# Kernel optimization log

Measured on AMD Instinct MI355X. Metric: run time of the kernel, lower is better.

The kernel has to match this reference:

```python
import jax, jax.numpy as jnp
import numpy as np

NEG_SLOPE = 0.2
BN_EPS = 1e-5
SM_EPS = 1e-16


def gatv2_conv(x, src, dst, num_nodes, Wl, bl, Wr, br, att, bias, concat):
    # x: [N, Fin]; att: [H, C]
    H, C = att.shape
    xl = (x @ Wl + bl).reshape(-1, H, C)  # source-side (x_j), lin_l
    xr = (x @ Wr + br).reshape(-1, H, C)  # target-side (x_i), lin_r
    e = jax.nn.leaky_relu(xl[src] + xr[dst], NEG_SLOPE)          # [E, H, C]
    logits = jnp.einsum('ehc,hc->eh', e, att)                    # [E, H]
    m = jax.ops.segment_max(logits, dst, num_segments=num_nodes)  # [N, H]
    expv = jnp.exp(logits - m[dst])
    denom = jax.ops.segment_sum(expv, dst, num_segments=num_nodes)
    alpha = expv / (denom[dst] + SM_EPS)                          # [E, H]
    msg = xl[src] * alpha[:, :, None]                             # [E, H, C]
    out = jax.ops.segment_sum(msg, dst, num_segments=num_nodes)   # [N, H, C]
    out = out.reshape(num_nodes, H * C) if concat else out.mean(axis=1)
    return out + bias


def batchnorm(x, gamma, beta):
    mean = x.mean(axis=0)
    var = x.var(axis=0)  # biased, as torch uses for normalization
    return gamma * (x - mean) * jax.lax.rsqrt(var + BN_EPS) + beta


def setup_inputs() -> dict:
    key = jax.random.key(0)
    ks = jax.random.split(key, 16)
    N, E = 50000, 800000
    Fin, Hid, Out, H = 128, 64, 64, 4
    s = 0.05
    inp = {
        'x': jax.random.normal(ks[0], (N, Fin), jnp.float32),
        'edge_index': jax.random.randint(ks[1], (2, E), 0, N, jnp.int64),
        # conv1 (heads=4, concat=False)
        'Wl1': jax.random.normal(ks[2], (Fin, H * Hid), jnp.float32) * s,
        'bl1': jnp.zeros((H * Hid,), jnp.float32),
        'Wr1': jax.random.normal(ks[3], (Fin, H * Hid), jnp.float32) * s,
        'br1': jnp.zeros((H * Hid,), jnp.float32),
        'att1': jax.random.normal(ks[4], (H, Hid), jnp.float32) * s,
        'bias1': jnp.zeros((Hid,), jnp.float32),
        'g1': jnp.ones((Hid,), jnp.float32),
        'beta1': jnp.zeros((Hid,), jnp.float32),
        # conv2 (heads=1, concat=True -> same as single head)
        'Wl2': jax.random.normal(ks[5], (Hid, Out), jnp.float32) * s,
        'bl2': jnp.zeros((Out,), jnp.float32),
        'Wr2': jax.random.normal(ks[6], (Hid, Out), jnp.float32) * s,
        'br2': jnp.zeros((Out,), jnp.float32),
        'att2': jax.random.normal(ks[7], (1, Out), jnp.float32) * s,
        'bias2': jnp.zeros((Out,), jnp.float32),
        'g2': jnp.ones((Out,), jnp.float32),
        'beta2': jnp.zeros((Out,), jnp.float32),
    }
    return inp


def reference(x, edge_index, Wl1, bl1, Wr1, br1, att1, bias1, g1, beta1,
              Wl2, bl2, Wr2, br2, att2, bias2, g2, beta2):
    N = x.shape[0]
    loops = jnp.arange(N, dtype=edge_index.dtype)  # PyG add_self_loops=True
    src = jnp.concatenate([edge_index[0], loops])
    dst = jnp.concatenate([edge_index[1], loops])
    h = gatv2_conv(x, src, dst, N, Wl1, bl1, Wr1, br1, att1, bias1, concat=False)
    h = jax.nn.relu(batchnorm(h, g1, beta1))  # dropout = identity (eval)
    h = gatv2_conv(h, src, dst, N, Wl2, bl2, Wr2, br2, att2, bias2, concat=True)
    h = jax.nn.relu(batchnorm(h, g2, beta2))
    return h
```

## Files before the change

kernel.cpp:

```cpp
#include <hip/hip_runtime.h>
#include <hip/hip_bf16.h>
#include <math.h>

#define TPB 256

typedef __attribute__((ext_vector_type(8))) short bfrag8;
typedef __attribute__((ext_vector_type(4))) float f32x4;

static __device__ __forceinline__ float bf2f(unsigned int u) {
  union { unsigned int i; float f; } c; c.i = u << 16; return c.f;
}
static __device__ __forceinline__ unsigned short f2bf(float f) {
  union { float f; unsigned int i; } c; c.f = f;
  unsigned int lsb = (c.i >> 16) & 1u;
  return (unsigned short)((c.i + 0x7fffu + lsb) >> 16);
}

__global__ void k_deg(const int* __restrict__ ei, int E, int ET, int* __restrict__ deg) {
  int e = blockIdx.x * blockDim.x + threadIdx.x;
  if (e >= ET) return;
  int dst = (e < E) ? ei[E + e] : (e - E);
  atomicAdd(&deg[dst], 1);
}

__global__ void k_scan1(const int* __restrict__ deg, int N, int* __restrict__ bsum) {
  __shared__ int sm[TPB];
  int i = blockIdx.x * TPB + threadIdx.x;
  sm[threadIdx.x] = (i < N) ? deg[i] : 0;
  __syncthreads();
  for (int d = TPB / 2; d > 0; d >>= 1) {
    if (threadIdx.x < d) sm[threadIdx.x] += sm[threadIdx.x + d];
    __syncthreads();
  }
  if (threadIdx.x == 0) bsum[blockIdx.x] = sm[0];
}

__global__ void k_scan3(const int* __restrict__ deg, const int* __restrict__ bsum,
                        int SB, int N, int* __restrict__ rowoff, int* __restrict__ cursor) {
  __shared__ int sm[TPB];
  int pv = (threadIdx.x < blockIdx.x) ? bsum[threadIdx.x] : 0;
  sm[threadIdx.x] = pv;
  __syncthreads();
  for (int dd = TPB / 2; dd > 0; dd >>= 1) {
    if (threadIdx.x < dd) sm[threadIdx.x] += sm[threadIdx.x + dd];
    __syncthreads();
  }
  int base = sm[0];
  __syncthreads();
  int i = blockIdx.x * TPB + threadIdx.x;
  int v = (i < N) ? deg[i] : 0;
  sm[threadIdx.x] = v;
  __syncthreads();
  for (int dd = 1; dd < TPB; dd <<= 1) {
    int t = (threadIdx.x >= dd) ? sm[threadIdx.x - dd] : 0;
    __syncthreads();
    sm[threadIdx.x] += t;
    __syncthreads();
  }
  if (i < N) {
    int off = base + sm[threadIdx.x] - v;
    rowoff[i] = off;
    cursor[i] = off;
  }
  if (blockIdx.x == SB - 1 && threadIdx.x == TPB - 1) rowoff[N] = base + sm[TPB - 1];
}

__global__ void k_fill(const int* __restrict__ ei, int E, int ET,
                       int* __restrict__ cursor, int* __restrict__ csrc) {
  int e = blockIdx.x * blockDim.x + threadIdx.x;
  if (e >= ET) return;
  int src, dst;
  if (e < E) { src = ei[e]; dst = ei[E + e]; } else { src = dst = e - E; }
  int pos = atomicAdd(&cursor[dst], 1);
  csrc[pos] = src;
}

__global__ void k_prep1(const float* __restrict__ x,
                        const float* __restrict__ Wl1, const float* __restrict__ Wr1,
                        const float* __restrict__ Wl2, const float* __restrict__ Wr2,
                        unsigned short* __restrict__ xb,
                        unsigned short* __restrict__ wt1l, unsigned short* __restrict__ wt1r,
                        unsigned short* __restrict__ wt2l, unsigned short* __restrict__ wt2r,
                        int nx4) {
  int i = blockIdx.x * blockDim.x + threadIdx.x;
  int stride = gridDim.x * blockDim.x;
  int wtot = nx4 + 65536 + 8192;
  for (; i < wtot; i += stride) {
    if (i < nx4) {
      float4 v = *(const float4*)(x + (size_t)i * 4);
      ushort4 o; o.x = f2bf(v.x); o.y = f2bf(v.y); o.z = f2bf(v.z); o.w = f2bf(v.w);
      *(ushort4*)(xb + (size_t)i * 4) = o;
    } else if (i < nx4 + 32768) {
      int j = i - nx4; int c = j >> 7, k = j & 127;
      wt1l[j] = f2bf(Wl1[(size_t)k * 256 + c]);
    } else if (i < nx4 + 65536) {
      int j = i - nx4 - 32768; int c = j >> 7, k = j & 127;
      wt1r[j] = f2bf(Wr1[(size_t)k * 256 + c]);
    } else if (i < nx4 + 65536 + 4096) {
      int j = i - nx4 - 65536; int c = j >> 6, k = j & 63;
      wt2l[j] = f2bf(Wl2[(size_t)k * 64 + c]);
    } else {
      int j = i - nx4 - 69632; int c = j >> 6, k = j & 63;
      wt2r[j] = f2bf(Wr2[(size_t)k * 64 + c]);
    }
  }
}

__global__ void k_prep2(const float* __restrict__ in, const float* __restrict__ ab,
                        unsigned short* __restrict__ o, int n4) {
  int i = blockIdx.x * blockDim.x + threadIdx.x;
  if (i >= n4) return;
  float4 v = *(const float4*)(in + (size_t)i * 4);
  int c0 = (i & 15) * 4;
  ushort4 u;
  u.x = f2bf(fmaxf(v.x * ab[c0 + 0] + ab[64 + c0 + 0], 0.f));
  u.y = f2bf(fmaxf(v.y * ab[c0 + 1] + ab[64 + c0 + 1], 0.f));
  u.z = f2bf(fmaxf(v.z * ab[c0 + 2] + ab[64 + c0 + 2], 0.f));
  u.w = f2bf(fmaxf(v.w * ab[c0 + 3] + ab[64 + c0 + 3], 0.f));
  *(ushort4*)(o + (size_t)i * 4) = u;
}

__global__ void k_gemm_mfma(const unsigned short* __restrict__ Ab,
                            const unsigned short* __restrict__ Wt0, const float* __restrict__ b0,
                            const unsigned short* __restrict__ Wt1, const float* __restrict__ b1,
                            const float* __restrict__ att,
                            float* __restrict__ dl, float* __restrict__ dr,
                            unsigned short* __restrict__ out0, unsigned short* __restrict__ out1,
                            int M, int K, int Nc, int Hs) {
  extern __shared__ short lds[];
  short* As = lds;
  short* Bls = lds + 64 * K;
  short* Brs = lds + 128 * K;
  const int r0 = blockIdx.x * 64, n0 = blockIdx.y * 64;
  const int tid = threadIdx.x;
  const int Kb = K * 2;
  const int cpr = K >> 3;
  const int chunks = 64 * cpr;
  for (int idx = tid; idx < chunks; idx += TPB) {
    int row = idx / cpr, k8 = (idx - row * cpr) * 8;
    int kb = (k8 * 2) ^ ((row & 7) << 4);
    int gr = r0 + row;
    uint4 av = make_uint4(0, 0, 0, 0);
    if (gr < M) av = *(const uint4*)(Ab + (size_t)gr * K + k8);
    *(uint4*)((char*)As + row * Kb + kb) = av;
    uint4 w0 = *(const uint4*)(Wt0 + (size_t)(n0 + row) * K + k8);
    *(uint4*)((char*)Bls + row * Kb + kb) = w0;
    uint4 w1 = *(const uint4*)(Wt1 + (size_t)(n0 + row) * K + k8);
    *(uint4*)((char*)Brs + row * Kb + kb) = w1;
  }
  __syncthreads();

  const int w = tid >> 6, lane = tid & 63;
  const int arow = w * 16 + (lane & 15);
  const int l16 = (lane >> 4) << 3;
  f32x4 accL[4], accR[4];
#pragma unroll
  for (int i = 0; i < 4; ++i) { accL[i] = (f32x4)0.f; accR[i] = (f32x4)0.f; }
  for (int k0 = 0; k0 < K; k0 += 32) {
    int kb = (k0 + l16) * 2;
    bfrag8 af = *(bfrag8*)((char*)As + arow * Kb + (kb ^ ((arow & 7) << 4)));
#pragma unroll
    for (int cf = 0; cf < 4; ++cf) {
      int col = cf * 16 + (lane & 15);
      int cb = col * Kb + (kb ^ ((col & 7) << 4));
      bfrag8 bl = *(bfrag8*)((char*)Bls + cb);
      accL[cf] = __builtin_amdgcn_mfma_f32_16x16x32_bf16(af, bl, accL[cf], 0, 0, 0);
      bfrag8 br = *(bfrag8*)((char*)Brs + cb);
      accR[cf] = __builtin_amdgcn_mfma_f32_16x16x32_bf16(af, br, accR[cf], 0, 0, 0);
    }
  }
  const int rbase = r0 + w * 16 + ((lane >> 4) << 2);
  const int cbase = n0 + (lane & 15);
  float tL[4] = {0.f, 0.f, 0.f, 0.f}, tR[4] = {0.f, 0.f, 0.f, 0.f};
#pragma unroll
  for (int cf = 0; cf < 4; ++cf) {
    int gcol = cbase + cf * 16;
    float bb0 = b0[gcol], bb1 = b1[gcol], aa = att[gcol];
#pragma unroll
    for (int r = 0; r < 4; ++r) {
      float oL = accL[cf][r] + bb0, oR = accR[cf][r] + bb1;
      int grow = rbase + r;
      if (grow < M) {
        out0[(size_t)grow * Nc + gcol] = f2bf(oL);
        out1[(size_t)grow * Nc + gcol] = f2bf(oR);
      }
      tL[r] += oL * aa;
      tR[r] += oR * aa;
    }
  }
#pragma unroll
  for (int r = 0; r < 4; ++r) {
#pragma unroll
    for (int d = 1; d < 16; d <<= 1) {
      tL[r] += __shfl_xor(tL[r], d);
      tR[r] += __shfl_xor(tR[r], d);
    }
  }
  if ((lane & 15) == 0) {
    int h = n0 >> 6;
#pragma unroll
    for (int r = 0; r < 4; ++r) {
      int grow = rbase + r;
      if (grow < M) {
        dl[(size_t)grow * Hs + h] = 0.6f * tL[r];
        dr[(size_t)grow * Hs + h] = 0.6f * tR[r];
      }
    }
  }
}

__global__ void k_gat1(const unsigned short* __restrict__ xl,
                       const unsigned short* __restrict__ xr,
                       const float* __restrict__ dl, const float* __restrict__ dr,
                       const int* __restrict__ rowoff, const int* __restrict__ csrc,
                       const float* __restrict__ att, const float* __restrict__ bias,
                       float* __restrict__ out, int N, int nw) {
  int wid = (blockIdx.x * blockDim.x + threadIdx.x) >> 6;
  int lane = threadIdx.x & 63;
  int l4 = lane * 4, hid = lane >> 4;
  float4 atv = *(const float4*)(att + l4);
  float atx = 0.4f * atv.x, aty = 0.4f * atv.y, atz = 0.4f * atv.z, atw = 0.4f * atv.w;
  float4 bb = *(const float4*)(bias + l4);
  for (int node = wid; node < N; node += nw) {
    uint2 rv = *(const uint2*)(xr + (size_t)node * 256 + l4);
    float xr0 = bf2f(rv.x & 0xffffu), xr1 = bf2f(rv.x >> 16);
    float xr2 = bf2f(rv.y & 0xffffu), xr3 = bf2f(rv.y >> 16);
    float drv = dr[node * 4 + hid];
    int beg = rowoff[node], end = rowoff[node + 1];
    float s = 0.f, a0 = 0.f, a1 = 0.f, a2 = 0.f, a3 = 0.f;
    int k = beg;
    for (; k + 4 <= end; k += 4) {
      int srcs[4]; uint2 vv[4]; float dls[4], ps[4];
#pragma unroll
      for (int u = 0; u < 4; ++u) srcs[u] = csrc[k + u];
#pragma unroll
      for (int u = 0; u < 4; ++u) {
        vv[u] = *(const uint2*)(xl + (size_t)srcs[u] * 256 + l4);
        dls[u] = dl[srcs[u] * 4 + hid];
      }
#pragma unroll
      for (int u = 0; u < 4; ++u) {
        float x0 = bf2f(vv[u].x & 0xffffu), x1 = bf2f(vv[u].x >> 16);
        float x2 = bf2f(vv[u].y & 0xffffu), x3 = bf2f(vv[u].y >> 16);
        ps[u] = atx * fabsf(x0 + xr0) + aty * fabsf(x1 + xr1)
              + atz * fabsf(x2 + xr2) + atw * fabsf(x3 + xr3);
      }
#pragma unroll
      for (int u = 0; u < 4; ++u) {
        ps[u] += __shfl_xor(ps[u], 1); ps[u] += __shfl_xor(ps[u], 2);
        ps[u] += __shfl_xor(ps[u], 4); ps[u] += __shfl_xor(ps[u], 8);
      }
#pragma unroll
      for (int u = 0; u < 4; ++u) {
        float wv = __expf(ps[u] + dls[u] + drv);
        float x0 = bf2f(vv[u].x & 0xffffu), x1 = bf2f(vv[u].x >> 16);
        float x2 = bf2f(vv[u].y & 0xffffu), x3 = bf2f(vv[u].y >> 16);
        s += wv; a0 += wv * x0; a1 += wv * x1; a2 += wv * x2; a3 += wv * x3;
      }
    }
    if (k < end) {
      int srcs[4]; uint2 vv[4]; float dls[4], ps[4]; bool okv[4];
#pragma unroll
      for (int u = 0; u < 4; ++u) {
        okv[u] = (k + u) < end;
        srcs[u] = okv[u] ? csrc[k + u] : 0;
      }
#pragma unroll
      for (int u = 0; u < 4; ++u) {
        vv[u] = *(const uint2*)(xl + (size_t)srcs[u] * 256 + l4);
        dls[u] = dl[srcs[u] * 4 + hid];
      }
#pragma unroll
      for (int u = 0; u < 4; ++u) {
        float x0 = bf2f(vv[u].x & 0xffffu), x1 = bf2f(vv[u].x >> 16);
        float x2 = bf2f(vv[u].y & 0xffffu), x3 = bf2f(vv[u].y >> 16);
        ps[u] = atx * fabsf(x0 + xr0) + aty * fabsf(x1 + xr1)
              + atz * fabsf(x2 + xr2) + atw * fabsf(x3 + xr3);
      }
#pragma unroll
      for (int u = 0; u < 4; ++u) {
        ps[u] += __shfl_xor(ps[u], 1); ps[u] += __shfl_xor(ps[u], 2);
        ps[u] += __shfl_xor(ps[u], 4); ps[u] += __shfl_xor(ps[u], 8);
      }
#pragma unroll
      for (int u = 0; u < 4; ++u) {
        float wv = okv[u] ? __expf(ps[u] + dls[u] + drv) : 0.f;
        float x0 = bf2f(vv[u].x & 0xffffu), x1 = bf2f(vv[u].x >> 16);
        float x2 = bf2f(vv[u].y & 0xffffu), x3 = bf2f(vv[u].y >> 16);
        s += wv; a0 += wv * x0; a1 += wv * x1; a2 += wv * x2; a3 += wv * x3;
      }
    }
    float inv = 1.f / (s + 1e-16f);
    a0 *= inv; a1 *= inv; a2 *= inv; a3 *= inv;
    a0 += __shfl_xor(a0, 16); a0 += __shfl_xor(a0, 32);
    a1 += __shfl_xor(a1, 16); a1 += __shfl_xor(a1, 32);
    a2 += __shfl_xor(a2, 16); a2 += __shfl_xor(a2, 32);
    a3 += __shfl_xor(a3, 16); a3 += __shfl_xor(a3, 32);
    if (lane < 16) {
      float4 o;
      o.x = a0 * 0.25f + bb.x;
      o.y = a1 * 0.25f + bb.y;
      o.z = a2 * 0.25f + bb.z;
      o.w = a3 * 0.25f + bb.w;
      *(float4*)(out + (size_t)node * 64 + l4) = o;
    }
  }
}

__global__ void k_gat2(const unsigned short* __restrict__ xl,
                       const unsigned short* __restrict__ xr,
                       const float* __restrict__ dl, const float* __restrict__ dr,
                       const int* __restrict__ rowoff, const int* __restrict__ csrc,
                       const float* __restrict__ att, const float* __restrict__ bias,
                       float* __restrict__ out, int N, int nw) {
  int wid = (blockIdx.x * blockDim.x + threadIdx.x) >> 6;
  int lane = threadIdx.x & 63;
  int grp = lane >> 4, c4 = (lane & 15) * 4;
  float4 atv = *(const float4*)(att + c4);
  float atx = 0.4f * atv.x, aty = 0.4f * atv.y, atz = 0.4f * atv.z, atw = 0.4f * atv.w;
  float4 bb = *(const float4*)(bias + c4);
  for (int node = wid; node < N; node += nw) {
    uint2 rv = *(const uint2*)(xr + (size_t)node * 64 + c4);
    float xr0 = bf2f(rv.x & 0xffffu), xr1 = bf2f(rv.x >> 16);
    float xr2 = bf2f(rv.y & 0xffffu), xr3 = bf2f(rv.y >> 16);
    float drv = dr[node];
    int beg = rowoff[node], end = rowoff[node + 1];
    int nf = (end - beg) >> 2;
    float s = 0.f, a0 = 0.f, a1 = 0.f, a2 = 0.f, a3 = 0.f;
    for (int it = 0; it < nf; ++it) {
      int kk = beg + it * 4 + grp;
      int src = csrc[kk];
      float dlv = dl[src];
      uint2 v = *(const uint2*)(xl + (size_t)src * 64 + c4);
      float x0 = bf2f(v.x & 0xffffu), x1 = bf2f(v.x >> 16);
      float x2 = bf2f(v.y & 0xffffu), x3 = bf2f(v.y >> 16);
      float p = atx * fabsf(x0 + xr0) + aty * fabsf(x1 + xr1)
              + atz * fabsf(x2 + xr2) + atw * fabsf(x3 + xr3);
      p += __shfl_xor(p, 1); p += __shfl_xor(p, 2);
      p += __shfl_xor(p, 4); p += __shfl_xor(p, 8);
      float wv = __expf(p + dlv + drv);
      s += wv; a0 += wv * x0; a1 += wv * x1; a2 += wv * x2; a3 += wv * x3;
    }
    if ((end - beg) & 3) {
      int kk = beg + nf * 4 + grp;
      bool ok = kk < end;
      int src = ok ? csrc[kk] : 0;
      float dlv = dl[src];
      uint2 v = *(const uint2*)(xl + (size_t)src * 64 + c4);
      float x0 = bf2f(v.x & 0xffffu), x1 = bf2f(v.x >> 16);
      float x2 = bf2f(v.y & 0xffffu), x3 = bf2f(v.y >> 16);
      float p = atx * fabsf(x0 + xr0) + aty * fabsf(x1 + xr1)
              + atz * fabsf(x2 + xr2) + atw * fabsf(x3 + xr3);
      p += __shfl_xor(p, 1); p += __shfl_xor(p, 2);
      p += __shfl_xor(p, 4); p += __shfl_xor(p, 8);
      float wv = ok ? __expf(p + dlv + drv) : 0.f;
      s += wv; a0 += wv * x0; a1 += wv * x1; a2 += wv * x2; a3 += wv * x3;
    }
    s  += __shfl_xor(s, 16);  s  += __shfl_xor(s, 32);
    a0 += __shfl_xor(a0, 16); a0 += __shfl_xor(a0, 32);
    a1 += __shfl_xor(a1, 16); a1 += __shfl_xor(a1, 32);
    a2 += __shfl_xor(a2, 16); a2 += __shfl_xor(a2, 32);
    a3 += __shfl_xor(a3, 16); a3 += __shfl_xor(a3, 32);
    if (lane < 16) {
      float inv = 1.f / (s + 1e-16f);
      float4 o;
      o.x = a0 * inv + bb.x;
      o.y = a1 * inv + bb.y;
      o.z = a2 * inv + bb.z;
      o.w = a3 * inv + bb.w;
      *(float4*)(out + (size_t)node * 64 + c4) = o;
    }
  }
}

__global__ void k_bnstat(const float* __restrict__ in, int N, float* __restrict__ part) {
  __shared__ float sm[TPB], sq[TPB];
  int col = threadIdx.x & 63;
  int rq = threadIdx.x >> 6;
  float s = 0.f, q = 0.f;
  for (int r = blockIdx.x * 4 + rq; r < N; r += gridDim.x * 4) {
    float v = in[(size_t)r * 64 + col];
    s += v; q += v * v;
  }
  sm[threadIdx.x] = s; sq[threadIdx.x] = q;
  __syncthreads();
  if (threadIdx.x < 64) {
    s = sm[threadIdx.x] + sm[threadIdx.x + 64] + sm[threadIdx.x + 128] + sm[threadIdx.x + 192];
    q = sq[threadIdx.x] + sq[threadIdx.x + 64] + sq[threadIdx.x + 128] + sq[threadIdx.x + 192];
    part[(size_t)blockIdx.x * 128 + threadIdx.x] = s;
    part[(size_t)blockIdx.x * 128 + 64 + threadIdx.x] = q;
  }
}

__global__ void k_bnfin(const float* __restrict__ part, int B, int N,
                        const float* __restrict__ g, const float* __restrict__ beta,
                        float* __restrict__ ab) {
  int c = threadIdx.x;
  float s = 0.f, q = 0.f;
  for (int b = 0; b < B; ++b) {
    s += part[(size_t)b * 128 + c];
    q += part[(size_t)b * 128 + 64 + c];
  }
  float mean = s / (float)N;
  float var = q / (float)N - mean * mean;
  float a = g[c] * rsqrtf(var + 1e-5f);
  ab[c] = a;
  ab[64 + c] = beta[c] - mean * a;
}

__global__ void k_bnapply(const float* __restrict__ in, const float* __restrict__ ab,
                          float* __restrict__ out, int total4) {
  int idx = blockIdx.x * blockDim.x + threadIdx.x;
  if (idx >= total4) return;
  float4 v = *(const float4*)(in + (size_t)idx * 4);
  int c0 = (idx & 15) * 4;
  v.x = fmaxf(v.x * ab[c0 + 0] + ab[64 + c0 + 0], 0.f);
  v.y = fmaxf(v.y * ab[c0 + 1] + ab[64 + c0 + 1], 0.f);
  v.z = fmaxf(v.z * ab[c0 + 2] + ab[64 + c0 + 2], 0.f);
  v.w = fmaxf(v.w * ab[c0 + 3] + ab[64 + c0 + 3], 0.f);
  *(float4*)(out + (size_t)idx * 4) = v;
}

extern "C" void kernel_launch(void* const* d_in, const int* in_sizes, int n_in,
                              void* d_out, int out_size, void* d_ws, size_t ws_size,
                              hipStream_t stream) {
  const float* x     = (const float*)d_in[0];
  const int*   ei    = (const int*)d_in[1];
  const float* Wl1   = (const float*)d_in[2];
  const float* bl1   = (const float*)d_in[3];
  const float* Wr1   = (const float*)d_in[4];
  const float* br1   = (const float*)d_in[5];
  const float* att1  = (const float*)d_in[6];
  const float* bias1 = (const float*)d_in[7];
  const float* g1    = (const float*)d_in[8];
  const float* be1   = (const float*)d_in[9];
  const float* Wl2   = (const float*)d_in[10];
  const float* bl2   = (const float*)d_in[11];
  const float* Wr2   = (const float*)d_in[12];
  const float* br2   = (const float*)d_in[13];
  const float* att2  = (const float*)d_in[14];
  const float* bias2 = (const float*)d_in[15];
  const float* g2    = (const float*)d_in[16];
  const float* be2   = (const float*)d_in[17];
  float* out = (float*)d_out;

  const int N  = in_sizes[0] / 128;
  const int E  = in_sizes[1] / 2;
  const int ET = E + N;
  const int SB = (N + TPB - 1) / TPB;

  char* p = (char*)d_ws;
  auto take = [&](size_t b) { char* q = p; p += (b + 255) & ~(size_t)255; return q; };

  unsigned short* xl1 = (unsigned short*)take((size_t)N * 256 * 2);
  unsigned short* xr1 = (unsigned short*)take((size_t)N * 256 * 2);
  unsigned short* xl2 = (unsigned short*)take((size_t)N * 64 * 2);
  unsigned short* xr2 = (unsigned short*)take((size_t)N * 64 * 2);
  float* out1 = (float*)take((size_t)N * 64 * 4);
  unsigned short* xb = (unsigned short*)take((size_t)N * 128 * 2);
  unsigned short* wt1l = (unsigned short*)take(256 * 128 * 2);
  unsigned short* wt1r = (unsigned short*)take(256 * 128 * 2);
  unsigned short* wt2l = (unsigned short*)take(64 * 64 * 2);
  unsigned short* wt2r = (unsigned short*)take(64 * 64 * 2);
  float* dl1 = (float*)take((size_t)N * 4 * 4);
  float* dr1 = (float*)take((size_t)N * 4 * 4);
  float* dl2 = (float*)take((size_t)N * 4);
  float* dr2 = (float*)take((size_t)N * 4);
  int* deg    = (int*)take((size_t)N * 4);
  int* rowoff = (int*)take((size_t)(N + 1) * 4);
  int* cursor = (int*)take((size_t)N * 4);
  int* csrc   = (int*)take((size_t)ET * 4);
  int* bsum   = (int*)take((size_t)SB * 4);
  float* part = (float*)take((size_t)128 * 128 * 4);
  float* ab1  = (float*)take(128 * 4);
  float* ab2  = (float*)take(128 * 4);
  (void)ws_size; (void)n_in; (void)out_size;

  unsigned short* A2 = xb;

  int egrid = (ET + TPB - 1) / TPB;
  int mtile = (N + 63) / 64;
  int total4 = N * 16;
  int nx4 = N * 32;
  int wtot = nx4 + 65536 + 8192;
  const int GATB = 2048, NW = GATB * (TPB / 64);

  hipMemsetAsync(deg, 0, (size_t)N * 4, stream);
  k_deg<<<egrid, TPB, 0, stream>>>(ei, E, ET, deg);
  k_scan1<<<SB, TPB, 0, stream>>>(deg, N, bsum);
  k_scan3<<<SB, TPB, 0, stream>>>(deg, bsum, SB, N, rowoff, cursor);
  k_fill<<<egrid, TPB, 0, stream>>>(ei, E, ET, cursor, csrc);

  k_prep1<<<(wtot + TPB - 1) / TPB, TPB, 0, stream>>>(x, Wl1, Wr1, Wl2, Wr2,
                                                      xb, wt1l, wt1r, wt2l, wt2r, nx4);

  k_gemm_mfma<<<dim3(mtile, 4), TPB, 3 * 64 * 128 * 2, stream>>>(
      xb, wt1l, bl1, wt1r, br1, att1, dl1, dr1, xl1, xr1, N, 128, 256, 4);
  k_gat1<<<GATB, TPB, 0, stream>>>(xl1, xr1, dl1, dr1, rowoff, csrc, att1, bias1, out1, N, NW);
  k_bnstat<<<128, TPB, 0, stream>>>(out1, N, part);
  k_bnfin<<<1, 64, 0, stream>>>(part, 128, N, g1, be1, ab1);

  k_prep2<<<(total4 + TPB - 1) / TPB, TPB, 0, stream>>>(out1, ab1, A2, total4);
  k_gemm_mfma<<<dim3(mtile, 1), TPB, 3 * 64 * 64 * 2, stream>>>(
      A2, wt2l, bl2, wt2r, br2, att2, dl2, dr2, xl2, xr2, N, 64, 64, 1);
  k_gat2<<<GATB, TPB, 0, stream>>>(xl2, xr2, dl2, dr2, rowoff, csrc, att2, bias2, out, N, NW);
  k_bnstat<<<128, TPB, 0, stream>>>(out, N, part);
  k_bnfin<<<1, 64, 0, stream>>>(part, 128, N, g2, be2, ab2);
  k_bnapply<<<(total4 + TPB - 1) / TPB, TPB, 0, stream>>>(out, ab2, out, total4);
}
```

Measured before the change: 405.1 us.

## Drop precomputed linear attention terms, compute leaky-relu directly with packed float2 math

Removes the algebraic split of leaky_relu into 0.6*linear + 0.4*abs terms, so the GEMM no longer computes and stores per-node dl/dr attention dot products and the GAT kernels stop gathering dl per edge. The leaky-relu is evaluated directly with max(t, 0.2t) using float2 vectors, which may map to packed FP32 instructions. The GAT kernels also switch from a grid-stride loop over 2048 blocks to one wave per node with a full grid. This cuts one scattered load per edge and the GEMM epilogue reduction, at the cost of slightly more ALU work per edge and many more launched blocks.

```diff
diff --git a/kernel.cpp b/kernel.cpp
--- a/kernel.cpp
+++ b/kernel.cpp
@@ -6,9 +6,16 @@
 
 typedef __attribute__((ext_vector_type(8))) short bfrag8;
 typedef __attribute__((ext_vector_type(4))) float f32x4;
+typedef __attribute__((ext_vector_type(2))) float f32x2;
 
 static __device__ __forceinline__ float bf2f(unsigned int u) {
   union { unsigned int i; float f; } c; c.i = u << 16; return c.f;
+}
+static __device__ __forceinline__ f32x2 unpk2(unsigned int u) {
+  union { unsigned int i; float f; } lo, hi;
+  lo.i = u << 16;
+  hi.i = u & 0xffff0000u;
+  f32x2 r; r.x = lo.f; r.y = hi.f; return r;
 }
 static __device__ __forceinline__ unsigned short f2bf(float f) {
   union { float f; unsigned int i; } c; c.f = f;
@@ -123,10 +130,8 @@
 __global__ void k_gemm_mfma(const unsigned short* __restrict__ Ab,
                             const unsigned short* __restrict__ Wt0, const float* __restrict__ b0,
                             const unsigned short* __restrict__ Wt1, const float* __restrict__ b1,
-                            const float* __restrict__ att,
-                            float* __restrict__ dl, float* __restrict__ dr,
                             unsigned short* __restrict__ out0, unsigned short* __restrict__ out1,
-                            int M, int K, int Nc, int Hs) {
+                            int M, int K, int Nc) {
   extern __shared__ short lds[];
   short* As = lds;
   short* Bls = lds + 64 * K;
@@ -171,39 +176,16 @@
   }
   const int rbase = r0 + w * 16 + ((lane >> 4) << 2);
   const int cbase = n0 + (lane & 15);
-  float tL[4] = {0.f, 0.f, 0.f, 0.f}, tR[4] = {0.f, 0.f, 0.f, 0.f};
 #pragma unroll
   for (int cf = 0; cf < 4; ++cf) {
     int gcol = cbase + cf * 16;
-    float bb0 = b0[gcol], bb1 = b1[gcol], aa = att[gcol];
-#pragma unroll
-    for (int r = 0; r < 4; ++r) {
-      float oL = accL[cf][r] + bb0, oR = accR[cf][r] + bb1;
-      int grow = rbase + r;
-      if (grow < M) {
-        out0[(size_t)grow * Nc + gcol] = f2bf(oL);
-        out1[(size_t)grow * Nc + gcol] = f2bf(oR);
-      }
-      tL[r] += oL * aa;
-      tR[r] += oR * aa;
-    }
-  }
-#pragma unroll
-  for (int r = 0; r < 4; ++r) {
-#pragma unroll
-    for (int d = 1; d < 16; d <<= 1) {
-      tL[r] += __shfl_xor(tL[r], d);
-      tR[r] += __shfl_xor(tR[r], d);
-    }
-  }
-  if ((lane & 15) == 0) {
-    int h = n0 >> 6;
+    float bb0 = b0[gcol], bb1 = b1[gcol];
 #pragma unroll
     for (int r = 0; r < 4; ++r) {
       int grow = rbase + r;
       if (grow < M) {
-        dl[(size_t)grow * Hs + h] = 0.6f * tL[r];
-        dr[(size_t)grow * Hs + h] = 0.6f * tR[r];
+        out0[(size_t)grow * Nc + gcol] = f2bf(accL[cf][r] + bb0);
+        out1[(size_t)grow * Nc + gcol] = f2bf(accR[cf][r] + bb1);
       }
     }
   }
@@ -211,165 +193,157 @@
 
 __global__ void k_gat1(const unsigned short* __restrict__ xl,
                        const unsigned short* __restrict__ xr,
-                       const float* __restrict__ dl, const float* __restrict__ dr,
                        const int* __restrict__ rowoff, const int* __restrict__ csrc,
                        const float* __restrict__ att, const float* __restrict__ bias,
-                       float* __restrict__ out, int N, int nw) {
-  int wid = (blockIdx.x * blockDim.x + threadIdx.x) >> 6;
+                       float* __restrict__ out, int N) {
+  int node = (blockIdx.x * blockDim.x + threadIdx.x) >> 6;
   int lane = threadIdx.x & 63;
-  int l4 = lane * 4, hid = lane >> 4;
+  if (node >= N) return;
+  int l4 = lane * 4;
   float4 atv = *(const float4*)(att + l4);
-  float atx = 0.4f * atv.x, aty = 0.4f * atv.y, atz = 0.4f * atv.z, atw = 0.4f * atv.w;
+  f32x2 at01; at01.x = atv.x; at01.y = atv.y;
+  f32x2 at23; at23.x = atv.z; at23.y = atv.w;
   float4 bb = *(const float4*)(bias + l4);
-  for (int node = wid; node < N; node += nw) {
-    uint2 rv = *(const uint2*)(xr + (size_t)node * 256 + l4);
-    float xr0 = bf2f(rv.x & 0xffffu), xr1 = bf2f(rv.x >> 16);
-    float xr2 = bf2f(rv.y & 0xffffu), xr3 = bf2f(rv.y >> 16);
-    float drv = dr[node * 4 + hid];
-    int beg = rowoff[node], end = rowoff[node + 1];
-    float s = 0.f, a0 = 0.f, a1 = 0.f, a2 = 0.f, a3 = 0.f;
-    int k = beg;
-    for (; k + 4 <= end; k += 4) {
-      int srcs[4]; uint2 vv[4]; float dls[4], ps[4];
-#pragma unroll
-      for (int u = 0; u < 4; ++u) srcs[u] = csrc[k + u];
-#pragma unroll
-      for (int u = 0; u < 4; ++u) {
-        vv[u] = *(const uint2*)(xl + (size_t)srcs[u] * 256 + l4);
-        dls[u] = dl[srcs[u] * 4 + hid];
-      }
-#pragma unroll
-      for (int u = 0; u < 4; ++u) {
-        float x0 = bf2f(vv[u].x & 0xffffu), x1 = bf2f(vv[u].x >> 16);
-        float x2 = bf2f(vv[u].y & 0xffffu), x3 = bf2f(vv[u].y >> 16);
-        ps[u] = atx * fabsf(x0 + xr0) + aty * fabsf(x1 + xr1)
-              + atz * fabsf(x2 + xr2) + atw * fabsf(x3 + xr3);
-      }
-#pragma unroll
-      for (int u = 0; u < 4; ++u) {
-        ps[u] += __shfl_xor(ps[u], 1); ps[u] += __shfl_xor(ps[u], 2);
-        ps[u] += __shfl_xor(ps[u], 4); ps[u] += __shfl_xor(ps[u], 8);
-      }
-#pragma unroll
-      for (int u = 0; u < 4; ++u) {
-        float wv = __expf(ps[u] + dls[u] + drv);
-        float x0 = bf2f(vv[u].x & 0xffffu), x1 = bf2f(vv[u].x >> 16);
-        float x2 = bf2f(vv[u].y & 0xffffu), x3 = bf2f(vv[u].y >> 16);
-        s += wv; a0 += wv * x0; a1 += wv * x1; a2 += wv * x2; a3 += wv * x3;
-      }
-    }
-    if (k < end) {
-      int srcs[4]; uint2 vv[4]; float dls[4], ps[4]; bool okv[4];
-#pragma unroll
-      for (int u = 0; u < 4; ++u) {
-        okv[u] = (k + u) < end;
-        srcs[u] = okv[u] ? csrc[k + u] : 0;
-      }
-#pragma unroll
-      for (int u = 0; u < 4; ++u) {
-        vv[u] = *(const uint2*)(xl + (size_t)srcs[u] * 256 + l4);
-        dls[u] = dl[srcs[u] * 4 + hid];
-      }
-#pragma unroll
-      for (int u = 0; u < 4; ++u) {
-        float x0 = bf2f(vv[u].x & 0xffffu), x1 = bf2f(vv[u].x >> 16);
-        float x2 = bf2f(vv[u].y & 0xffffu), x3 = bf2f(vv[u].y >> 16);
-        ps[u] = atx * fabsf(x0 + xr0) + aty * fabsf(x1 + xr1)
-              + atz * fabsf(x2 + xr2) + atw * fabsf(x3 + xr3);
-      }
-#pragma unroll
-      for (int u = 0; u < 4; ++u) {
-        ps[u] += __shfl_xor(ps[u], 1); ps[u] += __shfl_xor(ps[u], 2);
-        ps[u] += __shfl_xor(ps[u], 4); ps[u] += __shfl_xor(ps[u], 8);
-      }
-#pragma unroll
-      for (int u = 0; u < 4; ++u) {
-        float wv = okv[u] ? __expf(ps[u] + dls[u] + drv) : 0.f;
-        float x0 = bf2f(vv[u].x & 0xffffu), x1 = bf2f(vv[u].x >> 16);
-        float x2 = bf2f(vv[u].y & 0xffffu), x3 = bf2f(vv[u].y >> 16);
-        s += wv; a0 += wv * x0; a1 += wv * x1; a2 += wv * x2; a3 += wv * x3;
-      }
-    }
-    float inv = 1.f / (s + 1e-16f);
-    a0 *= inv; a1 *= inv; a2 *= inv; a3 *= inv;
-    a0 += __shfl_xor(a0, 16); a0 += __shfl_xor(a0, 32);
-    a1 += __shfl_xor(a1, 16); a1 += __shfl_xor(a1, 32);
-    a2 += __shfl_xor(a2, 16); a2 += __shfl_xor(a2, 32);
-    a3 += __shfl_xor(a3, 16); a3 += __shfl_xor(a3, 32);
-    if (lane < 16) {
-      float4 o;
-      o.x = a0 * 0.25f + bb.x;
-      o.y = a1 * 0.25f + bb.y;
-      o.z = a2 * 0.25f + bb.z;
-      o.w = a3 * 0.25f + bb.w;
-      *(float4*)(out + (size_t)node * 64 + l4) = o;
-    }
+  uint2 rv = *(const uint2*)(xr + (size_t)node * 256 + l4);
+  f32x2 xr01 = unpk2(rv.x), xr23 = unpk2(rv.y);
+  int beg = rowoff[node], end = rowoff[node + 1];
+  float s = 0.f;
+  f32x2 ac01 = {0.f, 0.f}, ac23 = {0.f, 0.f};
+  int k = beg;
+  for (; k + 4 <= end; k += 4) {
+    int srcs[4]; uint2 vv[4];
+#pragma unroll
+    for (int u = 0; u < 4; ++u) srcs[u] = csrc[k + u];
+#pragma unroll
+    for (int u = 0; u < 4; ++u) vv[u] = *(const uint2*)(xl + (size_t)srcs[u] * 256 + l4);
+    f32x2 x01[4], x23[4]; float ps[4];
+#pragma unroll
+    for (int u = 0; u < 4; ++u) {
+      x01[u] = unpk2(vv[u].x); x23[u] = unpk2(vv[u].y);
+      f32x2 t01 = x01[u] + xr01, t23 = x23[u] + xr23;
+      f32x2 m01 = t01 * 0.2f, m23 = t23 * 0.2f;
+      f32x2 l01, l23;
+      l01.x = fmaxf(t01.x, m01.x); l01.y = fmaxf(t01.y, m01.y);
+      l23.x = fmaxf(t23.x, m23.x); l23.y = fmaxf(t23.y, m23.y);
+      f32x2 pf = at01 * l01 + at23 * l23;
+      ps[u] = pf.x + pf.y;
+    }
+#pragma unroll
+    for (int u = 0; u < 4; ++u) {
+      ps[u] += __shfl_xor(ps[u], 1); ps[u] += __shfl_xor(ps[u], 2);
+      ps[u] += __shfl_xor(ps[u], 4); ps[u] += __shfl_xor(ps[u], 8);
+    }
+#pragma unroll
+    for (int u = 0; u < 4; ++u) {
+      float wv = __expf(ps[u]);
+      s += wv;
+      ac01 += x01[u] * wv;
+      ac23 += x23[u] * wv;
+    }
+  }
+  if (k < end) {
+    int srcs[4]; uint2 vv[4]; bool okv[4];
+#pragma unroll
+    for (int u = 0; u < 4; ++u) {
+      okv[u] = (k + u) < end;
+      srcs[u] = okv[u] ? csrc[k + u] : 0;
+    }
+#pragma unroll
+    for (int u = 0; u < 4; ++u) vv[u] = *(const uint2*)(xl + (size_t)srcs[u] * 256 + l4);
+    f32x2 x01[4], x23[4]; float ps[4];
+#pragma unroll
+    for (int u = 0; u < 4; ++u) {
+      x01[u] = unpk2(vv[u].x); x23[u] = unpk2(vv[u].y);
+      f32x2 t01 = x01[u] + xr01, t23 = x23[u] + xr23;
+      f32x2 m01 = t01 * 0.2f, m23 = t23 * 0.2f;
+      f32x2 l01, l23;
+      l01.x = fmaxf(t01.x, m01.x); l01.y = fmaxf(t01.y, m01.y);
+      l23.x = fmaxf(t23.x, m23.x); l23.y = fmaxf(t23.y, m23.y);
+      f32x2 pf = at01 * l01 + at23 * l23;
+      ps[u] = pf.x + pf.y;
+    }
+#pragma unroll
+    for (int u = 0; u < 4; ++u) {
+      ps[u] += __shfl_xor(ps[u], 1); ps[u] += __shfl_xor(ps[u], 2);
+      ps[u] += __shfl_xor(ps[u], 4); ps[u] += __shfl_xor(ps[u], 8);
+    }
+#pragma unroll
+    for (int u = 0; u < 4; ++u) {
+      float wv = okv[u] ? __expf(ps[u]) : 0.f;
+      s += wv;
+      ac01 += x01[u] * wv;
+      ac23 += x23[u] * wv;
+    }
+  }
+  float inv = 1.f / (s + 1e-16f);
+  float a0 = ac01.x * inv, a1 = ac01.y * inv, a2 = ac23.x * inv, a3 = ac23.y * inv;
+  a0 += __shfl_xor(a0, 16); a0 += __shfl_xor(a0, 32);
+  a1 += __shfl_xor(a1, 16); a1 += __shfl_xor(a1, 32);
+  a2 += __shfl_xor(a2, 16); a2 += __shfl_xor(a2, 32);
+  a3 += __shfl_xor(a3, 16); a3 += __shfl_xor(a3, 32);
+  if (lane < 16) {
+    float4 o;
+    o.x = a0 * 0.25f + bb.x;
+    o.y = a1 * 0.25f + bb.y;
+    o.z = a2 * 0.25f + bb.z;
+    o.w = a3 * 0.25f + bb.w;
+    *(float4*)(out + (size_t)node * 64 + l4) = o;
   }
 }
 
 __global__ void k_gat2(const unsigned short* __restrict__ xl,
                        const unsigned short* __restrict__ xr,
-                       const float* __restrict__ dl, const float* __restrict__ dr,
                        const int* __restrict__ rowoff, const int* __restrict__ csrc,
                        const float* __restrict__ att, const float* __restrict__ bias,
-                       float* __restrict__ out, int N, int nw) {
-  int wid = (blockIdx.x * blockDim.x + threadIdx.x) >> 6;
+                       float* __restrict__ out, int N) {
+  int node = (blockIdx.x * blockDim.x + threadIdx.x) >> 6;
   int lane = threadIdx.x & 63;
+  if (node >= N) return;
   int grp = lane >> 4, c4 = (lane & 15) * 4;
   float4 atv = *(const float4*)(att + c4);
-  float atx = 0.4f * atv.x, aty = 0.4f * atv.y, atz = 0.4f * atv.z, atw = 0.4f * atv.w;
+  f32x2 at01; at01.x = atv.x; at01.y = atv.y;
+  f32x2 at23; at23.x = atv.z; at23.y = atv.w;
   float4 bb = *(const float4*)(bias + c4);
-  for (int node = wid; node < N; node += nw) {
-    uint2 rv = *(const uint2*)(xr + (size_t)node * 64 + c4);
-    float xr0 = bf2f(rv.x & 0xffffu), xr1 = bf2f(rv.x >> 16);
-    float xr2 = bf2f(rv.y & 0xffffu), xr3 = bf2f(rv.y >> 16);
-    float drv = dr[node];
-    int beg = rowoff[node], end = rowoff[node + 1];
-    int nf = (end - beg) >> 2;
-    float s = 0.f, a0 = 0.f, a1 = 0.f, a2 = 0.f, a3 = 0.f;
-    for (int it = 0; it < nf; ++it) {
-      int kk = beg + it * 4 + grp;
-      int src = csrc[kk];
-      float dlv = dl[src];
-      uint2 v = *(const uint2*)(xl + (size_t)src * 64 + c4);
-      float x0 = bf2f(v.x & 0xffffu), x1 = bf2f(v.x >> 16);
-      float x2 = bf2f(v.y & 0xffffu), x3 = bf2f(v.y >> 16);
-      float p = atx * fabsf(x0 + xr0) + aty * fabsf(x1 + xr1)
-              + atz * fabsf(x2 + xr2) + atw * fabsf(x3 + xr3);
-      p += __shfl_xor(p, 1); p += __shfl_xor(p, 2);
-      p += __shfl_xor(p, 4); p += __shfl_xor(p, 8);
-      float wv = __expf(p + dlv + drv);
-      s += wv; a0 += wv * x0; a1 += wv * x1; a2 += wv * x2; a3 += wv * x3;
-    }
-    if ((end - beg) & 3) {
-      int kk = beg + nf * 4 + grp;
-      bool ok = kk < end;
-      int src = ok ? csrc[kk] : 0;
-      float dlv = dl[src];
-      uint2 v = *(const uint2*)(xl + (size_t)src * 64 + c4);
-      float x0 = bf2f(v.x & 0xffffu), x1 = bf2f(v.x >> 16);
-      float x2 = bf2f(v.y & 0xffffu), x3 = bf2f(v.y >> 16);
-      float p = atx * fabsf(x0 + xr0) + aty * fabsf(x1 + xr1)
-              + atz * fabsf(x2 + xr2) + atw * fabsf(x3 + xr3);
-      p += __shfl_xor(p, 1); p += __shfl_xor(p, 2);
-      p += __shfl_xor(p, 4); p += __shfl_xor(p, 8);
-      float wv = ok ? __expf(p + dlv + drv) : 0.f;
-      s += wv; a0 += wv * x0; a1 += wv * x1; a2 += wv * x2; a3 += wv * x3;
-    }
-    s  += __shfl_xor(s, 16);  s  += __shfl_xor(s, 32);
-    a0 += __shfl_xor(a0, 16); a0 += __shfl_xor(a0, 32);
-    a1 += __shfl_xor(a1, 16); a1 += __shfl_xor(a1, 32);
-    a2 += __shfl_xor(a2, 16); a2 += __shfl_xor(a2, 32);
-    a3 += __shfl_xor(a3, 16); a3 += __shfl_xor(a3, 32);
-    if (lane < 16) {
-      float inv = 1.f / (s + 1e-16f);
-      float4 o;
-      o.x = a0 * inv + bb.x;
-      o.y = a1 * inv + bb.y;
-      o.z = a2 * inv + bb.z;
-      o.w = a3 * inv + bb.w;
-      *(float4*)(out + (size_t)node * 64 + c4) = o;
-    }
+  uint2 rv = *(const uint2*)(xr + (size_t)node * 64 + c4);
+  f32x2 xr01 = unpk2(rv.x), xr23 = unpk2(rv.y);
+  int beg = rowoff[node], end = rowoff[node + 1];
+  int iters = (end - beg + 3) >> 2;
+  float s = 0.f;
+  f32x2 ac01 = {0.f, 0.f}, ac23 = {0.f, 0.f};
+  for (int it = 0; it < iters; ++it) {
+    int kk = beg + it * 4 + grp;
+    bool ok = kk < end;
+    int src = ok ? csrc[kk] : 0;
+    uint2 v = *(const uint2*)(xl + (size_t)src * 64 + c4);
+    f32x2 x01 = unpk2(v.x), x23 = unpk2(v.y);
+    f32x2 t01 = x01 + xr01, t23 = x23 + xr23;
+    f32x2 m01 = t01 * 0.2f, m23 = t23 * 0.2f;
+    f32x2 l01, l23;
+    l01.x = fmaxf(t01.x, m01.x); l01.y = fmaxf(t01.y, m01.y);
+    l23.x = fmaxf(t23.x, m23.x); l23.y = fmaxf(t23.y, m23.y);
+    f32x2 pf = at01 * l01 + at23 * l23;
+    float p = pf.x + pf.y;
+    p += __shfl_xor(p, 1); p += __shfl_xor(p, 2);
+    p += __shfl_xor(p, 4); p += __shfl_xor(p, 8);
+    float wv = ok ? __expf(p) : 0.f;
+    s += wv;
+    ac01 += x01 * wv;
+    ac23 += x23 * wv;
+  }
+  s += __shfl_xor(s, 16); s += __shfl_xor(s, 32);
+  float a0 = ac01.x, a1 = ac01.y, a2 = ac23.x, a3 = ac23.y;
+  a0 += __shfl_xor(a0, 16); a0 += __shfl_xor(a0, 32);
+  a1 += __shfl_xor(a1, 16); a1 += __shfl_xor(a1, 32);
+  a2 += __shfl_xor(a2, 16); a2 += __shfl_xor(a2, 32);
+  a3 += __shfl_xor(a3, 16); a3 += __shfl_xor(a3, 32);
+  if (lane < 16) {
+    float inv = 1.f / (s + 1e-16f);
+    float4 o;
+    o.x = a0 * inv + bb.x;
+    o.y = a1 * inv + bb.y;
+    o.z = a2 * inv + bb.z;
+    o.w = a3 * inv + bb.w;
+    *(float4*)(out + (size_t)node * 64 + c4) = o;
   }
 }
 
@@ -462,10 +436,6 @@
   unsigned short* wt1r = (unsigned short*)take(256 * 128 * 2);
   unsigned short* wt2l = (unsigned short*)take(64 * 64 * 2);
   unsigned short* wt2r = (unsigned short*)take(64 * 64 * 2);
-  float* dl1 = (float*)take((size_t)N * 4 * 4);
-  float* dr1 = (float*)take((size_t)N * 4 * 4);
-  float* dl2 = (float*)take((size_t)N * 4);
-  float* dr2 = (float*)take((size_t)N * 4);
   int* deg    = (int*)take((size_t)N * 4);
   int* rowoff = (int*)take((size_t)(N + 1) * 4);
   int* cursor = (int*)take((size_t)N * 4);
@@ -479,11 +449,11 @@
   unsigned short* A2 = xb;
 
   int egrid = (ET + TPB - 1) / TPB;
+  int ngrid = (N + 3) / 4;
   int mtile = (N + 63) / 64;
   int total4 = N * 16;
   int nx4 = N * 32;
   int wtot = nx4 + 65536 + 8192;
-  const int GATB = 2048, NW = GATB * (TPB / 64);
 
   hipMemsetAsync(deg, 0, (size_t)N * 4, stream);
   k_deg<<<egrid, TPB, 0, stream>>>(ei, E, ET, deg);
@@ -495,15 +465,15 @@
                                                       xb, wt1l, wt1r, wt2l, wt2r, nx4);
 
   k_gemm_mfma<<<dim3(mtile, 4), TPB, 3 * 64 * 128 * 2, stream>>>(
-      xb, wt1l, bl1, wt1r, br1, att1, dl1, dr1, xl1, xr1, N, 128, 256, 4);
-  k_gat1<<<GATB, TPB, 0, stream>>>(xl1, xr1, dl1, dr1, rowoff, csrc, att1, bias1, out1, N, NW);
+      xb, wt1l, bl1, wt1r, br1, xl1, xr1, N, 128, 256);
+  k_gat1<<<ngrid, TPB, 0, stream>>>(xl1, xr1, rowoff, csrc, att1, bias1, out1, N);
   k_bnstat<<<128, TPB, 0, stream>>>(out1, N, part);
   k_bnfin<<<1, 64, 0, stream>>>(part, 128, N, g1, be1, ab1);
 
   k_prep2<<<(total4 + TPB - 1) / TPB, TPB, 0, stream>>>(out1, ab1, A2, total4);
   k_gemm_mfma<<<dim3(mtile, 1), TPB, 3 * 64 * 64 * 2, stream>>>(
-      A2, wt2l, bl2, wt2r, br2, att2, dl2, dr2, xl2, xr2, N, 64, 64, 1);
-  k_gat2<<<GATB, TPB, 0, stream>>>(xl2, xr2, dl2, dr2, rowoff, csrc, att2, bias2, out, N, NW);
+      A2, wt2l, bl2, wt2r, br2, xl2, xr2, N, 64, 64);
+  k_gat2<<<ngrid, TPB, 0, stream>>>(xl2, xr2, rowoff, csrc, att2, bias2, out, N);
   k_bnstat<<<128, TPB, 0, stream>>>(out, N, part);
   k_bnfin<<<1, 64, 0, stream>>>(part, 128, N, g2, be2, ab2);
   k_bnapply<<<(total4 + TPB - 1) / TPB, TPB, 0, stream>>>(out, ab2, out, total4);
```

Measured after the change: 389.8 us. -3.8%, faster.
